# Kernel tuning notes

Measured on AMD Instinct MI355X. Metric: run time of the kernel, lower is better.

Reference implementation:

```python
import jax, jax.numpy as jnp
import numpy as np

S, B, D, E, F = 2048, 2, 1024, 8, 4096


def setup_inputs() -> dict:
    key = jax.random.key(0)
    ks = jax.random.split(key, 6)
    x = jax.random.normal(ks[0], (S, B, D), dtype=jnp.float32)
    w_switch = jax.random.normal(ks[1], (D, E), dtype=jnp.float32) / np.sqrt(D)
    b_switch = jnp.zeros((E,), dtype=jnp.float32)
    w1 = jax.random.normal(ks[2], (E, D, F), dtype=jnp.float32) / np.sqrt(D)
    b1 = jnp.zeros((E, F), dtype=jnp.float32)
    w2 = jax.random.normal(ks[3], (E, F, D), dtype=jnp.float32) / np.sqrt(F)
    b2 = jnp.zeros((E, D), dtype=jnp.float32)
    return {"x": x, "w_switch": w_switch, "b_switch": b_switch,
            "w1": w1, "b1": b1, "w2": w2, "b2": b2}


def reference(x, w_switch, b_switch, w1, b1, w2, b2):
    # x: [S, B, D] -> tokens [N, D]
    s, b, d = x.shape
    n_experts = w1.shape[0]
    xf = x.reshape(-1, d)                                    # [N, D]
    route_prob = jax.nn.softmax(xf @ w_switch + b_switch, axis=-1)  # [N, E]
    route_prob_max = jnp.max(route_prob, axis=-1)            # [N]
    routes = jnp.argmax(route_prob, axis=-1)                 # [N] int
    # is_scale_prob=True: scale token by its routing probability before FFN
    xs = xf * route_prob_max[:, None]                        # [N, D]
    # Per-expert FFN evaluated densely (drop_tokens=False => every token kept),
    # then each token selects its routed expert's output.
    h = jax.nn.relu(jnp.einsum('nd,edf->enf', xs, w1) + b1[:, None, :])  # [E, N, F]
    y = jnp.einsum('enf,efd->end', h, w2) + b2[:, None, :]               # [E, N, D]
    n = xf.shape[0]
    out = y[routes, jnp.arange(n)]                           # [N, D]
    counts = jnp.zeros((n_experts,), dtype=jnp.float32).at[routes].add(1.0)
    n_dropped = jnp.zeros((), dtype=jnp.int32)               # drop_tokens=False
    return out.reshape(s, b, d), counts, route_prob.sum(0), n_dropped
```

## Files before the change

kernel.cpp:

```cpp
#include <hip/hip_runtime.h>
#include <hip/hip_bf16.h>

#define NTOK 4096
#define DDIM 1024
#define NEXP 8
#define FDIM 4096
#define MAXTILES 40

typedef __attribute__((ext_vector_type(4))) float f32x4;
typedef __attribute__((ext_vector_type(8))) short bf16x8;
typedef __attribute__((ext_vector_type(8))) unsigned short u16x8;

#define GLDS(g, l) __builtin_amdgcn_global_load_lds( \
    (const __attribute__((address_space(1))) unsigned int*)(g), \
    (__attribute__((address_space(3))) unsigned int*)(l), 16, 0, 0)

__global__ __launch_bounds__(256) void route_kernel(
    const float* __restrict__ x,
    const float* __restrict__ w_switch,
    const float* __restrict__ b_switch,
    __hip_bfloat16* __restrict__ xs,
    int* __restrict__ amax_arr,
    float* __restrict__ partial)
{
    const int tid = threadIdx.x;
    const int wave = tid >> 6, lane = tid & 63;
    __shared__ float pr[4][16];

    float wacc[16];
#pragma unroll
    for (int j = 0; j < 16; j++) wacc[j] = 0.0f;

    for (int i = 0; i < 4; i++) {
        const int n = blockIdx.x * 16 + wave * 4 + i;
        const float4* xr = (const float4*)(x + (size_t)n * DDIM);
        float4 xv[4];
#pragma unroll
        for (int j = 0; j < 4; j++) xv[j] = xr[lane + j * 64];

        float acc[NEXP];
#pragma unroll
        for (int e = 0; e < NEXP; e++) acc[e] = 0.0f;
#pragma unroll
        for (int j = 0; j < 4; j++) {
            const int dbase = (lane + j * 64) * 4;
#pragma unroll
            for (int c = 0; c < 4; c++) {
                const float4* wr = (const float4*)(w_switch + (size_t)(dbase + c) * NEXP);
                float4 w0 = wr[0], w1 = wr[1];
                float xvc = ((const float*)&xv[j])[c];
                acc[0] += xvc * w0.x; acc[1] += xvc * w0.y;
                acc[2] += xvc * w0.z; acc[3] += xvc * w0.w;
                acc[4] += xvc * w1.x; acc[5] += xvc * w1.y;
                acc[6] += xvc * w1.z; acc[7] += xvc * w1.w;
            }
        }
#pragma unroll
        for (int e = 0; e < NEXP; e++) {
            float v = acc[e];
#pragma unroll
            for (int off = 32; off > 0; off >>= 1) v += __shfl_xor(v, off, 64);
            acc[e] = v;
        }
        float mx = -1e30f;
#pragma unroll
        for (int e = 0; e < NEXP; e++) {
            acc[e] += b_switch[e];
            mx = fmaxf(mx, acc[e]);
        }
        float sum = 0.0f;
#pragma unroll
        for (int e = 0; e < NEXP; e++) { acc[e] = __expf(acc[e] - mx); sum += acc[e]; }
        float inv = 1.0f / sum;
        float pmax = -1.0f; int amax = 0;
#pragma unroll
        for (int e = 0; e < NEXP; e++) {
            float p = acc[e] * inv;
            acc[e] = p;
            if (p > pmax) { pmax = p; amax = e; }
        }
#pragma unroll
        for (int e = 0; e < NEXP; e++) {
            wacc[e] += acc[e];
            wacc[8 + e] += (amax == e) ? 1.0f : 0.0f;
        }
        if (lane == 0) amax_arr[n] = amax;
#pragma unroll
        for (int j = 0; j < 4; j++) {
            ushort4 pk;
            __hip_bfloat16* pp = (__hip_bfloat16*)&pk;
            pp[0] = __float2bfloat16(xv[j].x * pmax);
            pp[1] = __float2bfloat16(xv[j].y * pmax);
            pp[2] = __float2bfloat16(xv[j].z * pmax);
            pp[3] = __float2bfloat16(xv[j].w * pmax);
            *(ushort4*)(xs + (size_t)n * DDIM + (lane + j * 64) * 4) = pk;
        }
    }
    if (lane == 0) {
#pragma unroll
        for (int j = 0; j < 16; j++) pr[wave][j] = wacc[j];
    }
    __syncthreads();
    if (tid < 16)
        partial[blockIdx.x * 16 + tid] = pr[0][tid] + pr[1][tid] + pr[2][tid] + pr[3][tid];
}

__global__ __launch_bounds__(1024) void bucket_kernel(
    const int* __restrict__ amax_arr, int* __restrict__ bucket, int* __restrict__ ecnt)
{
    const int e = blockIdx.x;
    __shared__ int ctr;
    if (threadIdx.x == 0) ctr = 0;
    __syncthreads();
    const int lane = threadIdx.x & 63;
    for (int c = 0; c < NTOK; c += 1024) {
        int t = c + threadIdx.x;
        bool my = (amax_arr[t] == e);
        unsigned long long mask = __ballot(my);
        int cnt = __popcll(mask);
        int base = 0;
        if (lane == 0 && cnt) base = atomicAdd(&ctr, cnt);
        base = __shfl(base, 0, 64);
        if (my) {
            int rank = __popcll(mask & ((1ull << lane) - 1ull));
            bucket[e * NTOK + base + rank] = t;
        }
    }
    __syncthreads();
    if (threadIdx.x == 0) ecnt[e] = ctr;
}

__global__ __launch_bounds__(256) void finalize_table_kernel(
    const float* __restrict__ partial, const int* __restrict__ ecnt,
    float* __restrict__ out_tail, int* __restrict__ table)
{
    __shared__ float red[16][16];
    const int j = threadIdx.x & 15, g = threadIdx.x >> 4;
    float s = 0.0f;
    for (int k = 0; k < 16; k++) s += partial[(size_t)(g + k * 16) * 16 + j];
    red[g][j] = s;
    __syncthreads();
    if (threadIdx.x < 16) {
        float t = 0.0f;
        for (int k = 0; k < 16; k++) t += red[k][threadIdx.x];
        int dst = (threadIdx.x < 8) ? (8 + threadIdx.x) : (threadIdx.x - 8);
        out_tail[dst] = t;
    }
    if (threadIdx.x == 16) out_tail[16] = 0.0f;
    if (threadIdx.x == 0) {
        int idx = 0;
        for (int e = 0; e < NEXP; e++) {
            int cnt = ecnt[e];
            for (int m0 = 0; m0 < cnt; m0 += 128) table[idx++] = (e << 16) | m0;
        }
        for (; idx < MAXTILES; idx++) table[idx] = -1;
    }
}

__global__ __launch_bounds__(256) void init_out_kernel(
    const float* __restrict__ b2, const int* __restrict__ amax_arr,
    float* __restrict__ out)
{
    const int t = blockIdx.x;
    const int e = amax_arr[t];
    const float4* br = (const float4*)(b2 + (size_t)e * DDIM);
    ((float4*)(out + (size_t)t * DDIM))[threadIdx.x] = br[threadIdx.x];
}

template <int R, int C>
__global__ __launch_bounds__(256) void transpose_kernel(
    const float* __restrict__ in, __hip_bfloat16* __restrict__ outp)
{
    const int e = blockIdx.z;
    const int r0 = blockIdx.y * 64, c0 = blockIdx.x * 64;
    __shared__ __hip_bfloat16 t[64 * 65];
    const int tid = threadIdx.x;
    const int ri = tid >> 4, c4 = (tid & 15) * 4;
    const float* src = in + ((size_t)e * R + r0) * C + c0;
#pragma unroll
    for (int rr = 0; rr < 4; rr++) {
        int r = ri + rr * 16;
        float4 v = *(const float4*)(src + (size_t)r * C + c4);
        t[r * 65 + c4 + 0] = __float2bfloat16(v.x);
        t[r * 65 + c4 + 1] = __float2bfloat16(v.y);
        t[r * 65 + c4 + 2] = __float2bfloat16(v.z);
        t[r * 65 + c4 + 3] = __float2bfloat16(v.w);
    }
    __syncthreads();
    const int co = tid >> 2, m = tid & 3;
    u16x8 v0, v1;
#pragma unroll
    for (int idx = 0; idx < 8; idx++)
        ((unsigned short*)&v0)[idx] = *(const unsigned short*)&t[(m * 16 + idx) * 65 + co];
#pragma unroll
    for (int idx = 0; idx < 8; idx++)
        ((unsigned short*)&v1)[idx] = *(const unsigned short*)&t[(m * 16 + idx + 8) * 65 + co];
    __hip_bfloat16* dst = outp + ((size_t)e * C + c0 + co) * R + r0 + m * 16;
    *(u16x8*)(dst) = v0;
    *(u16x8*)(dst + 8) = v1;
}

template <int MODE, int K, int NN, int KS>
__device__ __forceinline__ void gemm_body(
    const __hip_bfloat16* __restrict__ A,
    const __hip_bfloat16* __restrict__ Bt,
    const float* __restrict__ bias,
    const int* __restrict__ bucket,
    const int* __restrict__ ecnt,
    const int* __restrict__ table,
    void* __restrict__ Out)
{
    const int entry = table[blockIdx.y];
    if (entry < 0) return;
    const int e = entry >> 16;
    const int m0 = entry & 0xffff;
    const int cnt = ecnt[e];
    const int n0 = blockIdx.x * 128;
    const int kbase = (K / KS) * blockIdx.z;

    __shared__ __align__(16) __hip_bfloat16 Asm[128 * 32];
    __shared__ __align__(16) __hip_bfloat16 Bsm[128 * 32];
    __shared__ int toks[128];

    const int tid = threadIdx.x;
    if (tid < 128) {
        int r = m0 + tid;
        toks[tid] = bucket[e * NTOK + (r < cnt ? r : cnt - 1)];
    }
    __syncthreads();

    const int wave = tid >> 6, lane = tid & 63;
    const int r = lane & 15, kq = lane >> 4;
    const int g0 = 2 * wave, g1 = 2 * wave + 1;

    const __hip_bfloat16* pA0 = A + (size_t)toks[g0 * 16 + r] * K + kbase + kq * 8;
    const __hip_bfloat16* pA1 = A + (size_t)toks[g1 * 16 + r] * K + kbase + kq * 8;
    const __hip_bfloat16* pB0 = Bt + ((size_t)e * NN + n0 + g0 * 16 + r) * K + kbase + kq * 8;
    const __hip_bfloat16* pB1 = Bt + ((size_t)e * NN + n0 + g1 * 16 + r) * K + kbase + kq * 8;
    char* lA0 = (char*)Asm + g0 * 1024;
    char* lA1 = (char*)Asm + g1 * 1024;
    char* lB0 = (char*)Bsm + g0 * 1024;
    char* lB1 = (char*)Bsm + g1 * 1024;

    const int wm = wave & 1, wn = wave >> 1;
    f32x4 acc[4][4];
#pragma unroll
    for (int t = 0; t < 4; t++)
#pragma unroll
        for (int u = 0; u < 4; u++) acc[t][u] = (f32x4){0.f, 0.f, 0.f, 0.f};

    for (int k0 = 0; k0 < K / KS; k0 += 32) {
        GLDS(pA0, lA0); GLDS(pA1, lA1);
        GLDS(pB0, lB0); GLDS(pB1, lB1);
        pA0 += 32; pA1 += 32; pB0 += 32; pB1 += 32;
        __syncthreads();
        bf16x8 a[4], b[4];
#pragma unroll
        for (int t = 0; t < 4; t++)
            a[t] = *(const bf16x8*)((const char*)Asm + (wm * 4 + t) * 1024 + lane * 16);
#pragma unroll
        for (int u = 0; u < 4; u++)
            b[u] = *(const bf16x8*)((const char*)Bsm + (wn * 4 + u) * 1024 + lane * 16);
#pragma unroll
        for (int t = 0; t < 4; t++)
#pragma unroll
            for (int u = 0; u < 4; u++)
                acc[t][u] = __builtin_amdgcn_mfma_f32_16x16x32_bf16(a[t], b[u], acc[t][u], 0, 0, 0);
        __syncthreads();
    }

    const int quad = lane >> 4, l15 = lane & 15;
    float bv[4];
#pragma unroll
    for (int u = 0; u < 4; u++)
        bv[u] = (MODE == 0) ? bias[(size_t)e * NN + n0 + wn * 64 + u * 16 + l15] : 0.0f;
#pragma unroll
    for (int t = 0; t < 4; t++) {
#pragma unroll
        for (int rr = 0; rr < 4; rr++) {
            int row = wm * 64 + t * 16 + quad * 4 + rr;
            if (m0 + row < cnt) {
                int tok = toks[row];
#pragma unroll
                for (int u = 0; u < 4; u++) {
                    int col = n0 + wn * 64 + u * 16 + l15;
                    float v = acc[t][u][rr] + bv[u];
                    if (MODE == 0) {
                        v = fmaxf(v, 0.0f);
                        ((__hip_bfloat16*)Out)[(size_t)tok * NN + col] = __float2bfloat16(v);
                    } else {
                        unsafeAtomicAdd(&((float*)Out)[(size_t)tok * NN + col], v);
                    }
                }
            }
        }
    }
}

__global__ __launch_bounds__(256) void gemm_ffn1(
    const __hip_bfloat16* __restrict__ A, const __hip_bfloat16* __restrict__ Bt,
    const float* __restrict__ bias, const int* __restrict__ bucket,
    const int* __restrict__ ecnt, const int* __restrict__ table, void* __restrict__ Out)
{
    gemm_body<0, DDIM, FDIM, 1>(A, Bt, bias, bucket, ecnt, table, Out);
}

__global__ __launch_bounds__(256) void gemm_ffn2(
    const __hip_bfloat16* __restrict__ A, const __hip_bfloat16* __restrict__ Bt,
    const float* __restrict__ bias, const int* __restrict__ bucket,
    const int* __restrict__ ecnt, const int* __restrict__ table, void* __restrict__ Out)
{
    gemm_body<1, FDIM, DDIM, 2>(A, Bt, bias, bucket, ecnt, table, Out);
}

extern "C" void kernel_launch(void* const* d_in, const int* in_sizes, int n_in,
                              void* d_out, int out_size, void* d_ws, size_t ws_size,
                              hipStream_t stream) {
    const float* x        = (const float*)d_in[0];
    const float* w_switch = (const float*)d_in[1];
    const float* b_switch = (const float*)d_in[2];
    const float* w1       = (const float*)d_in[3];
    const float* b1       = (const float*)d_in[4];
    const float* w2       = (const float*)d_in[5];
    const float* b2       = (const float*)d_in[6];

    float* out = (float*)d_out;
    float* out_tail = out + (size_t)NTOK * DDIM;

    char* ws = (char*)d_ws;
    __hip_bfloat16* xs = (__hip_bfloat16*)(ws);
    __hip_bfloat16* h  = (__hip_bfloat16*)(ws + 8388608ull);
    __hip_bfloat16* wt = (__hip_bfloat16*)(ws + 41943040ull);
    int* bucket        = (int*)(ws + 109051904ull);
    int* amax_arr      = (int*)(ws + 109182976ull);
    float* partial     = (float*)(ws + 109199360ull);
    int* ecnt          = (int*)(ws + 109215744ull);
    int* table         = (int*)(ws + 109215776ull);

    hipLaunchKernelGGL(route_kernel, dim3(256), dim3(256), 0, stream,
                       x, w_switch, b_switch, xs, amax_arr, partial);
    hipLaunchKernelGGL(bucket_kernel, dim3(NEXP), dim3(1024), 0, stream,
                       amax_arr, bucket, ecnt);
    hipLaunchKernelGGL(finalize_table_kernel, dim3(1), dim3(256), 0, stream,
                       partial, ecnt, out_tail, table);
    hipLaunchKernelGGL(init_out_kernel, dim3(NTOK), dim3(256), 0, stream,
                       b2, amax_arr, out);

    hipLaunchKernelGGL((transpose_kernel<DDIM, FDIM>), dim3(FDIM / 64, DDIM / 64, NEXP),
                       dim3(256), 0, stream, w1, wt);
    hipLaunchKernelGGL(gemm_ffn1, dim3(FDIM / 128, MAXTILES), dim3(256), 0, stream,
                       xs, wt, b1, bucket, ecnt, table, (void*)h);

    hipLaunchKernelGGL((transpose_kernel<FDIM, DDIM>), dim3(DDIM / 64, FDIM / 64, NEXP),
                       dim3(256), 0, stream, w2, wt);
    hipLaunchKernelGGL(gemm_ffn2, dim3(DDIM / 128, MAXTILES, 2), dim3(256), 0, stream,
                       h, wt, b2, bucket, ecnt, table, (void*)out);
}
```

Before: 529.5 us.

## Fuse weight transpose and bf16 cast into grouped GEMM B-tile loading

Removes the two separate transpose kernels that converted fp32 expert weights to transposed bf16, and instead has the GEMM load fp32 weights directly, convert to bf16 in registers and write them into LDS in MFMA layout. The main loop becomes double-buffered with register prefetch of the next B tile. The grid is reordered so tile entries vary fastest, and FFN2 split-K rises from 2 to 4. This saves the transpose round trip through memory but doubles B-operand global bytes per GEMM, since fp32 is read, and adds conversion work inside the loop. FFN2 also does more atomic adds into the output.

```diff
diff --git a/kernel.cpp b/kernel.cpp
--- a/kernel.cpp
+++ b/kernel.cpp
@@ -167,65 +167,34 @@
     ((float4*)(out + (size_t)t * DDIM))[threadIdx.x] = br[threadIdx.x];
 }
 
-template <int R, int C>
-__global__ __launch_bounds__(256) void transpose_kernel(
-    const float* __restrict__ in, __hip_bfloat16* __restrict__ outp)
-{
-    const int e = blockIdx.z;
-    const int r0 = blockIdx.y * 64, c0 = blockIdx.x * 64;
-    __shared__ __hip_bfloat16 t[64 * 65];
-    const int tid = threadIdx.x;
-    const int ri = tid >> 4, c4 = (tid & 15) * 4;
-    const float* src = in + ((size_t)e * R + r0) * C + c0;
-#pragma unroll
-    for (int rr = 0; rr < 4; rr++) {
-        int r = ri + rr * 16;
-        float4 v = *(const float4*)(src + (size_t)r * C + c4);
-        t[r * 65 + c4 + 0] = __float2bfloat16(v.x);
-        t[r * 65 + c4 + 1] = __float2bfloat16(v.y);
-        t[r * 65 + c4 + 2] = __float2bfloat16(v.z);
-        t[r * 65 + c4 + 3] = __float2bfloat16(v.w);
-    }
-    __syncthreads();
-    const int co = tid >> 2, m = tid & 3;
-    u16x8 v0, v1;
-#pragma unroll
-    for (int idx = 0; idx < 8; idx++)
-        ((unsigned short*)&v0)[idx] = *(const unsigned short*)&t[(m * 16 + idx) * 65 + co];
-#pragma unroll
-    for (int idx = 0; idx < 8; idx++)
-        ((unsigned short*)&v1)[idx] = *(const unsigned short*)&t[(m * 16 + idx + 8) * 65 + co];
-    __hip_bfloat16* dst = outp + ((size_t)e * C + c0 + co) * R + r0 + m * 16;
-    *(u16x8*)(dst) = v0;
-    *(u16x8*)(dst + 8) = v1;
-}
-
 template <int MODE, int K, int NN, int KS>
 __device__ __forceinline__ void gemm_body(
     const __hip_bfloat16* __restrict__ A,
-    const __hip_bfloat16* __restrict__ Bt,
+    const float* __restrict__ Bw,
     const float* __restrict__ bias,
     const int* __restrict__ bucket,
     const int* __restrict__ ecnt,
     const int* __restrict__ table,
     void* __restrict__ Out)
 {
-    const int entry = table[blockIdx.y];
+    const int entry = table[blockIdx.x];
     if (entry < 0) return;
     const int e = entry >> 16;
     const int m0 = entry & 0xffff;
     const int cnt = ecnt[e];
-    const int n0 = blockIdx.x * 128;
-    const int kbase = (K / KS) * blockIdx.z;
-
-    __shared__ __align__(16) __hip_bfloat16 Asm[128 * 32];
-    __shared__ __align__(16) __hip_bfloat16 Bsm[128 * 32];
+    const int n0 = blockIdx.y * 128;
+    constexpr int KB = K / KS;
+    constexpr int ITERS = KB / 32;
+    const int kbase = KB * blockIdx.z;
+
+    __shared__ __align__(16) __hip_bfloat16 Asm[2][128 * 32];
+    __shared__ __align__(16) __hip_bfloat16 Bsm[2][128 * 32];
     __shared__ int toks[128];
 
     const int tid = threadIdx.x;
     if (tid < 128) {
-        int r = m0 + tid;
-        toks[tid] = bucket[e * NTOK + (r < cnt ? r : cnt - 1)];
+        int rr = m0 + tid;
+        toks[tid] = bucket[e * NTOK + (rr < cnt ? rr : cnt - 1)];
     }
     __syncthreads();
 
@@ -235,12 +204,11 @@
 
     const __hip_bfloat16* pA0 = A + (size_t)toks[g0 * 16 + r] * K + kbase + kq * 8;
     const __hip_bfloat16* pA1 = A + (size_t)toks[g1 * 16 + r] * K + kbase + kq * 8;
-    const __hip_bfloat16* pB0 = Bt + ((size_t)e * NN + n0 + g0 * 16 + r) * K + kbase + kq * 8;
-    const __hip_bfloat16* pB1 = Bt + ((size_t)e * NN + n0 + g1 * 16 + r) * K + kbase + kq * 8;
-    char* lA0 = (char*)Asm + g0 * 1024;
-    char* lA1 = (char*)Asm + g1 * 1024;
-    char* lB0 = (char*)Bsm + g0 * 1024;
-    char* lB1 = (char*)Bsm + g1 * 1024;
+
+    const int krow = (tid >> 5) * 4;
+    const int nc = (tid & 31) * 4;
+    const float* Bg = Bw + ((size_t)e * K + kbase) * NN + n0 + nc;
+    const int boff = (nc >> 4) * 1024 + ((krow >> 3) * 16 + (nc & 15)) * 16 + (krow & 7) * 2;
 
     const int wm = wave & 1, wn = wave >> 1;
     f32x4 acc[4][4];
@@ -249,18 +217,65 @@
 #pragma unroll
         for (int u = 0; u < 4; u++) acc[t][u] = (f32x4){0.f, 0.f, 0.f, 0.f};
 
-    for (int k0 = 0; k0 < K / KS; k0 += 32) {
-        GLDS(pA0, lA0); GLDS(pA1, lA1);
-        GLDS(pB0, lB0); GLDS(pB1, lB1);
-        pA0 += 32; pA1 += 32; pB0 += 32; pB1 += 32;
-        __syncthreads();
+    float4 bcur[4], bnxt[4];
+#pragma unroll
+    for (int j = 0; j < 4; j++)
+        bcur[j] = *(const float4*)&Bg[(size_t)(krow + j) * NN];
+
+    GLDS(pA0, (char*)Asm[0] + g0 * 1024);
+    GLDS(pA1, (char*)Asm[0] + g1 * 1024);
+    pA0 += 32; pA1 += 32;
+
+    {
+        char* bb = (char*)Bsm[0] + boff;
+#pragma unroll
+        for (int i2 = 0; i2 < 4; i2++) {
+            ushort4 pk;
+            __hip_bfloat16* pp = (__hip_bfloat16*)&pk;
+            pp[0] = __float2bfloat16(((float*)&bcur[0])[i2]);
+            pp[1] = __float2bfloat16(((float*)&bcur[1])[i2]);
+            pp[2] = __float2bfloat16(((float*)&bcur[2])[i2]);
+            pp[3] = __float2bfloat16(((float*)&bcur[3])[i2]);
+            *(ushort4*)(bb + i2 * 16) = pk;
+        }
+    }
+    if (ITERS > 1) {
+#pragma unroll
+        for (int j = 0; j < 4; j++)
+            bnxt[j] = *(const float4*)&Bg[(size_t)(32 + krow + j) * NN];
+    }
+    __syncthreads();
+
+    for (int it = 0; it < ITERS; it++) {
+        const int cur = it & 1, nxt = cur ^ 1;
+        if (it + 1 < ITERS) {
+            GLDS(pA0, (char*)Asm[nxt] + g0 * 1024);
+            GLDS(pA1, (char*)Asm[nxt] + g1 * 1024);
+            pA0 += 32; pA1 += 32;
+            char* bb = (char*)Bsm[nxt] + boff;
+#pragma unroll
+            for (int i2 = 0; i2 < 4; i2++) {
+                ushort4 pk;
+                __hip_bfloat16* pp = (__hip_bfloat16*)&pk;
+                pp[0] = __float2bfloat16(((float*)&bnxt[0])[i2]);
+                pp[1] = __float2bfloat16(((float*)&bnxt[1])[i2]);
+                pp[2] = __float2bfloat16(((float*)&bnxt[2])[i2]);
+                pp[3] = __float2bfloat16(((float*)&bnxt[3])[i2]);
+                *(ushort4*)(bb + i2 * 16) = pk;
+            }
+        }
+        if (it + 2 < ITERS) {
+#pragma unroll
+            for (int j = 0; j < 4; j++)
+                bnxt[j] = *(const float4*)&Bg[(size_t)((it + 2) * 32 + krow + j) * NN];
+        }
         bf16x8 a[4], b[4];
 #pragma unroll
         for (int t = 0; t < 4; t++)
-            a[t] = *(const bf16x8*)((const char*)Asm + (wm * 4 + t) * 1024 + lane * 16);
+            a[t] = *(const bf16x8*)((const char*)Asm[cur] + (wm * 4 + t) * 1024 + lane * 16);
 #pragma unroll
         for (int u = 0; u < 4; u++)
-            b[u] = *(const bf16x8*)((const char*)Bsm + (wn * 4 + u) * 1024 + lane * 16);
+            b[u] = *(const bf16x8*)((const char*)Bsm[cur] + (wn * 4 + u) * 1024 + lane * 16);
 #pragma unroll
         for (int t = 0; t < 4; t++)
 #pragma unroll
@@ -298,19 +313,19 @@
 }
 
 __global__ __launch_bounds__(256) void gemm_ffn1(
-    const __hip_bfloat16* __restrict__ A, const __hip_bfloat16* __restrict__ Bt,
+    const __hip_bfloat16* __restrict__ A, const float* __restrict__ Bw,
     const float* __restrict__ bias, const int* __restrict__ bucket,
     const int* __restrict__ ecnt, const int* __restrict__ table, void* __restrict__ Out)
 {
-    gemm_body<0, DDIM, FDIM, 1>(A, Bt, bias, bucket, ecnt, table, Out);
+    gemm_body<0, DDIM, FDIM, 1>(A, Bw, bias, bucket, ecnt, table, Out);
 }
 
 __global__ __launch_bounds__(256) void gemm_ffn2(
-    const __hip_bfloat16* __restrict__ A, const __hip_bfloat16* __restrict__ Bt,
+    const __hip_bfloat16* __restrict__ A, const float* __restrict__ Bw,
     const float* __restrict__ bias, const int* __restrict__ bucket,
     const int* __restrict__ ecnt, const int* __restrict__ table, void* __restrict__ Out)
 {
-    gemm_body<1, FDIM, DDIM, 2>(A, Bt, bias, bucket, ecnt, table, Out);
+    gemm_body<1, FDIM, DDIM, 4>(A, Bw, bias, bucket, ecnt, table, Out);
 }
 
 extern "C" void kernel_launch(void* const* d_in, const int* in_sizes, int n_in,
@@ -330,12 +345,11 @@
     char* ws = (char*)d_ws;
     __hip_bfloat16* xs = (__hip_bfloat16*)(ws);
     __hip_bfloat16* h  = (__hip_bfloat16*)(ws + 8388608ull);
-    __hip_bfloat16* wt = (__hip_bfloat16*)(ws + 41943040ull);
-    int* bucket        = (int*)(ws + 109051904ull);
-    int* amax_arr      = (int*)(ws + 109182976ull);
-    float* partial     = (float*)(ws + 109199360ull);
-    int* ecnt          = (int*)(ws + 109215744ull);
-    int* table         = (int*)(ws + 109215776ull);
+    int* bucket        = (int*)(ws + 41943040ull);
+    int* amax_arr      = (int*)(ws + 42074112ull);
+    float* partial     = (float*)(ws + 42090496ull);
+    int* ecnt          = (int*)(ws + 42106880ull);
+    int* table         = (int*)(ws + 42106912ull);
 
     hipLaunchKernelGGL(route_kernel, dim3(256), dim3(256), 0, stream,
                        x, w_switch, b_switch, xs, amax_arr, partial);
@@ -346,13 +360,9 @@
     hipLaunchKernelGGL(init_out_kernel, dim3(NTOK), dim3(256), 0, stream,
                        b2, amax_arr, out);
 
-    hipLaunchKernelGGL((transpose_kernel<DDIM, FDIM>), dim3(FDIM / 64, DDIM / 64, NEXP),
-                       dim3(256), 0, stream, w1, wt);
-    hipLaunchKernelGGL(gemm_ffn1, dim3(FDIM / 128, MAXTILES), dim3(256), 0, stream,
-                       xs, wt, b1, bucket, ecnt, table, (void*)h);
-
-    hipLaunchKernelGGL((transpose_kernel<FDIM, DDIM>), dim3(DDIM / 64, FDIM / 64, NEXP),
-                       dim3(256), 0, stream, w2, wt);
-    hipLaunchKernelGGL(gemm_ffn2, dim3(DDIM / 128, MAXTILES, 2), dim3(256), 0, stream,
-                       h, wt, b2, bucket, ecnt, table, (void*)out);
-}
+    hipLaunchKernelGGL(gemm_ffn1, dim3(MAXTILES, FDIM / 128), dim3(256), 0, stream,
+                       xs, w1, b1, bucket, ecnt, table, (void*)h);
+
+    hipLaunchKernelGGL(gemm_ffn2, dim3(MAXTILES, DDIM / 128, 4), dim3(256), 0, stream,
+                       h, w2, b2, bucket, ecnt, table, (void*)out);
+}
```

Measured after the change: 565.9 us. +6.9%, slower.
